# Optimization experiments

Hardware: AMD Instinct MI355X
Metric: run time of the kernel (lower is better)

## Reference

```python
import jax, jax.numpy as jnp
import numpy as np

F_DIM, HID, H, DQ, DV = 1024, 4096, 16, 64, 64
EPS = 1e-6

def layer_norm(x, w, b):
    mu = jnp.mean(x, axis=-1, keepdims=True)
    var = jnp.mean(jnp.square(x - mu), axis=-1, keepdims=True)
    return (x - mu) * jax.lax.rsqrt(var + EPS) * w + b

def setup_inputs() -> dict:
    key = jax.random.key(0)
    ks = jax.random.split(key, 8)
    s = 0.02
    return {
        'x': jax.random.normal(ks[0], (4, 2048, F_DIM), dtype=jnp.float32),
        'ln1_w': jnp.ones((F_DIM,), jnp.float32),
        'ln1_b': jnp.zeros((F_DIM,), jnp.float32),
        'wq_w': jax.random.normal(ks[1], (H * DQ, F_DIM), jnp.float32) * s,
        'wq_b': jnp.zeros((H * DQ,), jnp.float32),
        'wk_w': jax.random.normal(ks[2], (H * DQ, F_DIM), jnp.float32) * s,
        'wk_b': jnp.zeros((H * DQ,), jnp.float32),
        'wv_w': jax.random.normal(ks[3], (H * DV, F_DIM), jnp.float32) * s,
        'wv_b': jnp.zeros((H * DV,), jnp.float32),
        'fc_w': jax.random.normal(ks[4], (F_DIM, H * DV), jnp.float32) * s,
        'fc_b': jnp.zeros((F_DIM,), jnp.float32),
        'ln2_w': jnp.ones((F_DIM,), jnp.float32),
        'ln2_b': jnp.zeros((F_DIM,), jnp.float32),
        'fc1_w': jax.random.normal(ks[5], (HID, F_DIM), jnp.float32) * s,
        'fc1_b': jnp.zeros((HID,), jnp.float32),
        'fc2_w': jax.random.normal(ks[6], (F_DIM, HID), jnp.float32) * s,
        'fc2_b': jnp.zeros((F_DIM,), jnp.float32),
    }

def reference(x, ln1_w, ln1_b, wq_w, wq_b, wk_w, wk_b, wv_w, wv_b,
              fc_w, fc_b, ln2_w, ln2_b, fc1_w, fc1_b, fc2_w, fc2_b):
    B, S, _ = x.shape
    # --- pre-LN multi-head self-attention ---
    h = layer_norm(x, ln1_w, ln1_b)
    q = (h @ wq_w.T + wq_b).reshape(B, S, H, DQ).transpose(0, 2, 1, 3)  # [B,H,S,dq]
    k = (h @ wk_w.T + wk_b).reshape(B, S, H, DQ).transpose(0, 2, 1, 3)
    v = (h @ wv_w.T + wv_b).reshape(B, S, H, DV).transpose(0, 2, 1, 3)
    attn = jax.nn.softmax(jnp.einsum('bhqd,bhkd->bhqk', q, k) / jnp.sqrt(jnp.float32(DQ)), axis=-1)
    out = jnp.einsum('bhqk,bhkd->bhqd', attn, v).transpose(0, 2, 1, 3).reshape(B, S, H * DV)
    x = x + (out @ fc_w.T + fc_b)
    # --- pre-LN residual MLP ---
    h2 = layer_norm(x, ln2_w, ln2_b)
    ff = jax.nn.relu(h2 @ fc1_w.T + fc1_b) @ fc2_w.T + fc2_b
    return x + ff
```

## Files before the change

kernel.cpp:

```cpp
#include <hip/hip_runtime.h>

#define F_DIMC 1024
#define HIDC   4096
#define NH     16
#define SEQ    2048
#define BATCH  4
#define ROWS   (BATCH * SEQ)
#define MEG    (1u << 20)
#define QSCALE 0.18033688011112042f

typedef unsigned short u16t;
typedef __attribute__((ext_vector_type(8))) short short8;
typedef __attribute__((ext_vector_type(4))) float floatx4;
typedef __attribute__((address_space(1))) void gvoid_t;
typedef __attribute__((address_space(3))) void lvoid_t;
#define ASYNC16(g, l) __builtin_amdgcn_global_load_lds((gvoid_t*)(g), (lvoid_t*)(l), 16, 0, 0)

#if __has_builtin(__builtin_amdgcn_exp2f)
#define EXP2(x) __builtin_amdgcn_exp2f(x)
#else
#define EXP2(x) exp2f(x)
#endif

__device__ __forceinline__ u16t f2bf(float f) {
    union { float f; unsigned u; } v; v.f = f;
    unsigned r = v.u + 0x7fffu + ((v.u >> 16) & 1u);
    return (u16t)(r >> 16);
}
__device__ __forceinline__ unsigned fasu(float f) {
    union { float f; unsigned u; } v; v.f = f; return v.u;
}

__global__ __launch_bounds__(256) void ln_kernel(const float* __restrict__ x,
                                                 const float* __restrict__ w,
                                                 const float* __restrict__ b,
                                                 u16t* __restrict__ out) {
    const int row = blockIdx.x;
    const int t = threadIdx.x;
    const float* xp = x + (size_t)row * F_DIMC;

    float4 v = *(const float4*)(xp + t * 4);
    float s  = v.x + v.y + v.z + v.w;
    float ss = v.x * v.x + v.y * v.y + v.z * v.z + v.w * v.w;
    for (int off = 32; off; off >>= 1) {
        s  += __shfl_down(s, off);
        ss += __shfl_down(ss, off);
    }
    __shared__ float red[8];
    const int wid = t >> 6, lid = t & 63;
    if (lid == 0) { red[wid] = s; red[4 + wid] = ss; }
    __syncthreads();
    if (t == 0) {
        float S  = red[0] + red[1] + red[2] + red[3];
        float SS = red[4] + red[5] + red[6] + red[7];
        float mu  = S * (1.0f / F_DIMC);
        float var = SS * (1.0f / F_DIMC) - mu * mu;
        red[0] = mu;
        red[1] = rsqrtf(var + 1e-6f);
    }
    __syncthreads();
    const float mu = red[0], rs = red[1];

    float4 wv = *(const float4*)(w + t * 4);
    float4 bv = *(const float4*)(b + t * 4);
    ushort4 o = make_ushort4(f2bf((v.x - mu) * rs * wv.x + bv.x),
                             f2bf((v.y - mu) * rs * wv.y + bv.y),
                             f2bf((v.z - mu) * rs * wv.z + bv.z),
                             f2bf((v.w - mu) * rs * wv.w + bv.w));
    *(ushort4*)(out + (size_t)row * F_DIMC + t * 4) = o;
}

__global__ __launch_bounds__(256) void wconv_kernel(const float* __restrict__ w0,
        const float* __restrict__ w1, const float* __restrict__ w2,
        const float* __restrict__ w3, const float* __restrict__ w4,
        const float* __restrict__ w5, u16t* __restrict__ dst) {
    const size_t e = ((size_t)blockIdx.x * 256 + threadIdx.x) * 4;
    const float* src; size_t off;
    if      (e < 1 * MEG) { src = w0; off = e; }
    else if (e < 2 * MEG) { src = w1; off = e - 1 * MEG; }
    else if (e < 3 * MEG) { src = w2; off = e - 2 * MEG; }
    else if (e < 4 * MEG) { src = w3; off = e - 3 * MEG; }
    else if (e < 8 * MEG) { src = w4; off = e - 4 * MEG; }
    else                  { src = w5; off = e - 8 * MEG; }
    float4 f = *(const float4*)(src + off);
    *(ushort4*)(dst + e) = make_ushort4(f2bf(f.x), f2bf(f.y), f2bf(f.z), f2bf(f.w));
}

#define DP_CORE(Aq, Wq, Kdim)                                                  \
    __shared__ u16t As[3][128 * 64] __attribute__((aligned(16)));              \
    __shared__ u16t Bs[3][256 * 64] __attribute__((aligned(16)));              \
    const int t = threadIdx.x;                                                 \
    const int lane = t & 63;                                                   \
    const int wave = t >> 6;                                                   \
    const int wm = wave >> 2, wn = wave & 3;                                   \
    const int fm = lane & 15, fq = lane >> 4;                                  \
        \
    const int nwg = gridDim.x;                                                 \
    const int swzb = (blockIdx.x & 7) * (nwg >> 3) + (blockIdx.x >> 3);        \
    const int m0 = (swzb & 63) * 128;                \
    const int n0 = (swzb >> 6) * 256;                                          \
                \
    const u16t* ag[2]; int alo[2];                                             \
    _Pragma("unroll")                                                          \
    for (int i = 0; i < 2; ++i) {                                              \
        const int beta = i * 512 + t;                                          \
        const int r = beta >> 3, j = (beta & 7) ^ (r & 7);                     \
        ag[i] = (Aq) + (size_t)(m0 + r) * (Kdim) + j * 8;                      \
        alo[i] = beta * 8;                                                     \
    }                                                                          \
    const u16t* bg[4]; int blo[4];                                             \
    _Pragma("unroll")                                                          \
    for (int i = 0; i < 4; ++i) {                                              \
        const int beta = i * 512 + t;                                          \
        const int r = beta >> 3, j = (beta & 7) ^ (r & 7);                     \
        bg[i] = (Wq) + (size_t)(n0 + r) * (Kdim) + j * 8;                      \
        blo[i] = beta * 8;                                                     \
    }                                                                          \
                \
    int aoffk[2], boffk[2];                                                    \
    {                                                                          \
        const int ra0 = wm * 64 + fm, rb0 = wn * 64 + fm;                      \
        _Pragma("unroll")                                                      \
        for (int ks = 0; ks < 2; ++ks) {                                       \
            aoffk[ks] = ra0 * 64 + ((ks * 4 + fq) ^ (ra0 & 7)) * 8;            \
            boffk[ks] = rb0 * 64 + ((ks * 4 + fq) ^ (rb0 & 7)) * 8;            \
        }                                                                      \
    }                                                                          \
    const int NT = (Kdim) / 64;                                                \
                       \
    _Pragma("unroll")                                                          \
    for (int i = 0; i < 2; ++i) ASYNC16(ag[i], &As[0][alo[i]]);                \
    _Pragma("unroll")                                                          \
    for (int i = 0; i < 4; ++i) ASYNC16(bg[i], &Bs[0][blo[i]]);                \
    _Pragma("unroll")                                                          \
    for (int i = 0; i < 2; ++i) { ASYNC16(ag[i] + 64, &As[1][alo[i]]); ag[i] += 128; } \
    _Pragma("unroll")                                                          \
    for (int i = 0; i < 4; ++i) { ASYNC16(bg[i] + 64, &Bs[1][blo[i]]); bg[i] += 128; } \
    asm volatile("s_waitcnt vmcnt(6)" ::: "memory");         \
    __builtin_amdgcn_s_barrier();                                              \
    __builtin_amdgcn_sched_barrier(0);                                         \
    floatx4 acc[4][4] = {};                                                    \
    int sc = 0, ss = 2;                                                        \
    for (int tt = 0; tt < NT; ++tt) {                                          \
        const u16t* Ab = As[sc];                                               \
        const u16t* Bb = Bs[sc];                                               \
        if (tt + 2 < NT) {                \
            u16t* la = As[ss]; u16t* lb = Bs[ss];                              \
            _Pragma("unroll")                                                  \
            for (int i = 0; i < 2; ++i) { ASYNC16(ag[i], la + alo[i]); ag[i] += 64; } \
            _Pragma("unroll")                                                  \
            for (int i = 0; i < 4; ++i) { ASYNC16(bg[i], lb + blo[i]); bg[i] += 64; } \
        }                                                                      \
        short8 fb0[4], fa0[4], fb1[4], fa1[4];                                 \
        _Pragma("unroll")                                                      \
        for (int ni = 0; ni < 4; ++ni) fb0[ni] = *(const short8*)(Bb + boffk[0] + ni * 1024); \
        _Pragma("unroll")                                                      \
        for (int mi = 0; mi < 4; ++mi) fa0[mi] = *(const short8*)(Ab + aoffk[0] + mi * 1024); \
        _Pragma("unroll")                                                      \
        for (int ni = 0; ni < 4; ++ni) fb1[ni] = *(const short8*)(Bb + boffk[1] + ni * 1024); \
        _Pragma("unroll")                                                      \
        for (int mi = 0; mi < 4; ++mi) fa1[mi] = *(const short8*)(Ab + aoffk[1] + mi * 1024); \
        asm volatile("s_waitcnt lgkmcnt(8)" ::: "memory");   \
        __builtin_amdgcn_sched_barrier(0);                                     \
        __builtin_amdgcn_s_setprio(1);                                         \
        _Pragma("unroll")                                                      \
        for (int mi = 0; mi < 4; ++mi)                                         \
            _Pragma("unroll")                                                  \
            for (int ni = 0; ni < 4; ++ni)                                     \
                acc[mi][ni] = __builtin_amdgcn_mfma_f32_16x16x32_bf16(         \
                    fa0[mi], fb0[ni], acc[mi][ni], 0, 0, 0);                   \
        __builtin_amdgcn_s_setprio(0);                                         \
        asm volatile("s_waitcnt lgkmcnt(0)" ::: "memory");   \
        __builtin_amdgcn_sched_barrier(0);                                     \
                                       \
        if (tt + 2 < NT) { asm volatile("s_waitcnt vmcnt(6)" ::: "memory"); }  \
        else             { asm volatile("s_waitcnt vmcnt(0)" ::: "memory"); }  \
        __builtin_amdgcn_s_barrier();                                          \
        __builtin_amdgcn_sched_barrier(0);                                     \
        __builtin_amdgcn_s_setprio(1);                                         \
        _Pragma("unroll")                                                      \
        for (int mi = 0; mi < 4; ++mi)                                         \
            _Pragma("unroll")                                                  \
            for (int ni = 0; ni < 4; ++ni)                                     \
                acc[mi][ni] = __builtin_amdgcn_mfma_f32_16x16x32_bf16(         \
                    fa1[mi], fb1[ni], acc[mi][ni], 0, 0, 0);                   \
        __builtin_amdgcn_s_setprio(0);                                         \
        sc = sc == 2 ? 0 : sc + 1;                                             \
        ss = ss == 2 ? 0 : ss + 1;                                             \
    }

template <bool RELU, bool RES, bool BF16OUT>
__global__ __launch_bounds__(512, 2) void gemm_dp(const u16t* __restrict__ A,
                                                  const u16t* __restrict__ W,
                                                  const float* __restrict__ bias,
                                                  const float* res, void* Cout,
                                                  int N, int K) {
    DP_CORE(A, W, K)
    float bl[4];
#pragma unroll
    for (int ni = 0; ni < 4; ++ni) bl[ni] = bias[n0 + wn * 64 + ni * 16 + fm];
#pragma unroll
    for (int mi = 0; mi < 4; ++mi) {
#pragma unroll
        for (int ni = 0; ni < 4; ++ni) {
            const int col = n0 + wn * 64 + ni * 16 + fm;
#pragma unroll
            for (int r = 0; r < 4; ++r) {
                const int row = m0 + wm * 64 + mi * 16 + fq * 4 + r;
                const size_t off = (size_t)row * N + col;
                float c = acc[mi][ni][r] + bl[ni];
                if (RELU) c = fmaxf(c, 0.0f);
                if (RES)  c += res[off];
                if (BF16OUT) ((u16t*)Cout)[off] = f2bf(c);
                else         ((float*)Cout)[off] = c;
            }
        }
    }
}

__global__ __launch_bounds__(512, 2) void gemm_qkv(const u16t* __restrict__ A,
        const u16t* __restrict__ W,
        const float* __restrict__ wq_b, const float* __restrict__ wk_b,
        const float* __restrict__ wv_b,
        u16t* __restrict__ qb, u16t* __restrict__ kb, u16t* __restrict__ vtb) {
    DP_CORE(A, W, F_DIMC)
    const int which = n0 >> 10;
    const int nb = n0 & 1023;
    const float* bias = which == 0 ? wq_b : which == 1 ? wk_b : wv_b;
    float bl[4];
#pragma unroll
    for (int ni = 0; ni < 4; ++ni) bl[ni] = bias[nb + wn * 64 + ni * 16 + fm];

    if (which == 2) {
#pragma unroll
        for (int mi = 0; mi < 4; ++mi)
#pragma unroll
            for (int ni = 0; ni < 4; ++ni) {
                const int col = nb + wn * 64 + ni * 16 + fm;
                const int row0 = m0 + wm * 64 + mi * 16 + fq * 4;
                ushort4 pk = make_ushort4(f2bf(acc[mi][ni][0] + bl[ni]),
                                          f2bf(acc[mi][ni][1] + bl[ni]),
                                          f2bf(acc[mi][ni][2] + bl[ni]),
                                          f2bf(acc[mi][ni][3] + bl[ni]));
                *(ushort4*)(vtb + (size_t)col * ROWS + row0) = pk;
            }
    } else {
        u16t* dst = (which == 0) ? qb : kb;
        const float sc2 = (which == 0) ? QSCALE : 1.0f;
#pragma unroll
        for (int mi = 0; mi < 4; ++mi)
#pragma unroll
            for (int ni = 0; ni < 4; ++ni) {
                const int col = nb + wn * 64 + ni * 16 + fm;
#pragma unroll
                for (int r = 0; r < 4; ++r) {
                    const int row = m0 + wm * 64 + mi * 16 + fq * 4 + r;
                    dst[(size_t)row * F_DIMC + col] = f2bf((acc[mi][ni][r] + bl[ni]) * sc2);
                }
            }
    }
}

__global__ __launch_bounds__(256, 4) void attn_mfma(const u16t* __restrict__ qb,
        const u16t* __restrict__ kbuf, const u16t* __restrict__ vtb,
        u16t* __restrict__ ab) {
    __shared__ u16t Kt[2][64 * 64] __attribute__((aligned(16)));
    __shared__ u16t Vs[64 * 64] __attribute__((aligned(16)));
    __shared__ u16t QP[128 * 64] __attribute__((aligned(16)));

    const int t = threadIdx.x;
    const int lane = t & 63;
    const int wave = t >> 6;
    const int l15 = lane & 15, q4 = lane >> 4;
    const int q0 = blockIdx.x * 128;
    const int bh = blockIdx.y;
    const int b = bh >> 4, hh = bh & 15;

#pragma unroll
    for (int c = 0; c < 4; ++c) {
        const int beta = c * 256 + t;
        const int r = beta >> 3, o = (beta & 7) ^ (r & 7);
        ASYNC16(qb + (size_t)(b * SEQ + q0 + r) * F_DIMC + hh * 64 + o * 8,
                QP + beta * 8);
    }
    const u16t* kg = kbuf + (size_t)(b * SEQ) * F_DIMC + hh * 64;
    const u16t* vg = vtb + (size_t)(hh * 64) * ROWS + b * SEQ;

    const int sb0 = t, sb1 = t + 256;
    const int sr0 = sb0 >> 3, so0 = (sb0 & 7) ^ (sr0 & 7);
    const int sr1 = sb1 >> 3, so1 = (sb1 & 7) ^ (sr1 & 7);
    const u16t* kp0 = kg + (size_t)sr0 * F_DIMC + so0 * 8;
    const u16t* kp1 = kg + (size_t)sr1 * F_DIMC + so1 * 8;
    const u16t* vp0 = vg + (size_t)sr0 * ROWS + so0 * 8;
    const u16t* vp1 = vg + (size_t)sr1 * ROWS + so1 * 8;

    ASYNC16(kp0, Kt[0] + sb0 * 8);
    ASYNC16(kp1, Kt[0] + sb1 * 8);
    ASYNC16(vp0, Vs + sb0 * 8);
    ASYNC16(vp1, Vs + sb1 * 8);
    kp0 += 64 * F_DIMC; kp1 += 64 * F_DIMC; vp0 += 64; vp1 += 64;
    __syncthreads();

    short8 fqr[2][2];
#pragma unroll
    for (int mt = 0; mt < 2; ++mt)
#pragma unroll
        for (int ks = 0; ks < 2; ++ks) {
            const int m = wave * 32 + mt * 16 + l15;
            const int oct = ks * 4 + q4;
            fqr[mt][ks] = *(const short8*)(QP + (m * 8 + (oct ^ (m & 7))) * 8);
        }

    short8 ones;
#pragma unroll
    for (int i = 0; i < 8; ++i) ones[i] = (short)0x3F80;

    floatx4 oacc[2][4] = {};
    floatx4 lacc[2] = {};

    for (int it = 0; it < SEQ / 64; ++it) {
        if (it + 1 < SEQ / 64) {
            u16t* kd = Kt[(it + 1) & 1];
            ASYNC16(kp0, kd + sb0 * 8);
            ASYNC16(kp1, kd + sb1 * 8);
            kp0 += 64 * F_DIMC; kp1 += 64 * F_DIMC;
        }
        const u16t* kcur = Kt[it & 1];

        short8 fk[4][2];
#pragma unroll
        for (int nt = 0; nt < 4; ++nt)
#pragma unroll
            for (int ks = 0; ks < 2; ++ks) {
                const int kr = nt * 16 + l15;
                const int oct = ks * 4 + q4;
                fk[nt][ks] = *(const short8*)(kcur + (kr * 8 + (oct ^ (kr & 7))) * 8);
            }
        floatx4 st[2][4] = {};
#pragma unroll
        for (int mt = 0; mt < 2; ++mt)
#pragma unroll
            for (int nt = 0; nt < 4; ++nt) {
                st[mt][nt] = __builtin_amdgcn_mfma_f32_16x16x32_bf16(
                    fk[nt][0], fqr[mt][0], st[mt][nt], 0, 0, 0);
                st[mt][nt] = __builtin_amdgcn_mfma_f32_16x16x32_bf16(
                    fk[nt][1], fqr[mt][1], st[mt][nt], 0, 0, 0);
            }

#pragma unroll
        for (int mt = 0; mt < 2; ++mt)
#pragma unroll
            for (int nt = 0; nt < 4; ++nt) {
                const float p0 = EXP2(st[mt][nt][0]);
                const float p1 = EXP2(st[mt][nt][1]);
                const float p2 = EXP2(st[mt][nt][2]);
                const float p3 = EXP2(st[mt][nt][3]);
                const unsigned lo = __builtin_amdgcn_perm(fasu(p1), fasu(p0), 0x07060302u);
                const unsigned hi = __builtin_amdgcn_perm(fasu(p3), fasu(p2), 0x07060302u);
                const int m = wave * 32 + mt * 16 + l15;
                const int logb = nt * 2 + (q4 >> 1);
                *(uint2*)(QP + (m * 8 + (logb ^ (m & 7))) * 8 + (q4 & 1) * 4) =
                    make_uint2(lo, hi);
            }

        __syncthreads();

        short8 fp[2][2], fv[4][2];
#pragma unroll
        for (int mt = 0; mt < 2; ++mt)
#pragma unroll
            for (int ks = 0; ks < 2; ++ks) {
                const int m = wave * 32 + mt * 16 + l15;
                const int oct = ks * 4 + q4;
                fp[mt][ks] = *(const short8*)(QP + (m * 8 + (oct ^ (m & 7))) * 8);
            }
#pragma unroll
        for (int nd = 0; nd < 4; ++nd)
#pragma unroll
            for (int ks = 0; ks < 2; ++ks) {
                const int d = nd * 16 + l15;
                const int oct = ks * 4 + q4;
                fv[nd][ks] = *(const short8*)(Vs + (d * 8 + (oct ^ (d & 7))) * 8);
            }
#pragma unroll
        for (int mt = 0; mt < 2; ++mt) {
#pragma unroll
            for (int nd = 0; nd < 4; ++nd) {
                oacc[mt][nd] = __builtin_amdgcn_mfma_f32_16x16x32_bf16(
                    fp[mt][0], fv[nd][0], oacc[mt][nd], 0, 0, 0);
                oacc[mt][nd] = __builtin_amdgcn_mfma_f32_16x16x32_bf16(
                    fp[mt][1], fv[nd][1], oacc[mt][nd], 0, 0, 0);
            }
            lacc[mt] = __builtin_amdgcn_mfma_f32_16x16x32_bf16(
                fp[mt][0], ones, lacc[mt], 0, 0, 0);
            lacc[mt] = __builtin_amdgcn_mfma_f32_16x16x32_bf16(
                fp[mt][1], ones, lacc[mt], 0, 0, 0);
        }

        __syncthreads();
        if (it + 1 < SEQ / 64) {
            ASYNC16(vp0, Vs + sb0 * 8);
            ASYNC16(vp1, Vs + sb1 * 8);
            vp0 += 64; vp1 += 64;
        }
    }

#pragma unroll
    for (int mt = 0; mt < 2; ++mt) {
        floatx4 rinv;
#pragma unroll
        for (int r = 0; r < 4; ++r) rinv[r] = 1.0f / lacc[mt][r];
#pragma unroll
        for (int nd = 0; nd < 4; ++nd)
#pragma unroll
            for (int r = 0; r < 4; ++r) {
                const int row = b * SEQ + q0 + wave * 32 + mt * 16 + q4 * 4 + r;
                const int col = hh * 64 + nd * 16 + l15;
                ab[(size_t)row * F_DIMC + col] = f2bf(oacc[mt][nd][r] * rinv[r]);
            }
    }
}

extern "C" void kernel_launch(void* const* d_in, const int* in_sizes, int n_in,
                              void* d_out, int out_size, void* d_ws, size_t ws_size,
                              hipStream_t stream) {
    const float* x     = (const float*)d_in[0];
    const float* ln1_w = (const float*)d_in[1];
    const float* ln1_b = (const float*)d_in[2];
    const float* wq_w  = (const float*)d_in[3];
    const float* wq_b  = (const float*)d_in[4];
    const float* wk_w  = (const float*)d_in[5];
    const float* wk_b  = (const float*)d_in[6];
    const float* wv_w  = (const float*)d_in[7];
    const float* wv_b  = (const float*)d_in[8];
    const float* fc_w  = (const float*)d_in[9];
    const float* fc_b  = (const float*)d_in[10];
    const float* ln2_w = (const float*)d_in[11];
    const float* ln2_b = (const float*)d_in[12];
    const float* fc1_w = (const float*)d_in[13];
    const float* fc1_b = (const float*)d_in[14];
    const float* fc2_w = (const float*)d_in[15];
    const float* fc2_b = (const float*)d_in[16];

    float* out = (float*)d_out;
    u16t*  ws  = (u16t*)d_ws;

    u16t* wbuf = ws;
    u16t* bwqkv = wbuf;
    u16t* bwfc = wbuf + 3 * MEG;
    u16t* bwf1 = wbuf + 4 * MEG;
    u16t* bwf2 = wbuf + 8 * MEG;
    u16t* h    = wbuf + 12 * MEG;
    u16t* qb   = h + 8 * MEG;
    u16t* kb   = qb + 8 * MEG;
    u16t* vtb  = kb + 8 * MEG;
    u16t* ab   = vtb + 8 * MEG;
    u16t* ff   = qb;

    const dim3 blk(256);
    const dim3 blk512(512);
    const int gQKV = 64 * (3072 / 256);
    const int gF   = 64 * (F_DIMC / 256);
    const int gH   = 64 * (HIDC / 256);

    wconv_kernel<<<12 * MEG / 1024, blk, 0, stream>>>(wq_w, wk_w, wv_w, fc_w, fc1_w, fc2_w, wbuf);
    ln_kernel<<<ROWS, blk, 0, stream>>>(x, ln1_w, ln1_b, h);
    gemm_qkv<<<gQKV, blk512, 0, stream>>>(h, bwqkv, wq_b, wk_b, wv_b, qb, kb, vtb);
    attn_mfma<<<dim3(SEQ / 128, BATCH * NH), blk, 0, stream>>>(qb, kb, vtb, ab);
    gemm_dp<false, true, false><<<gF, blk512, 0, stream>>>(ab, bwfc, fc_b, x, out, F_DIMC, F_DIMC);
    ln_kernel<<<ROWS, blk, 0, stream>>>(out, ln2_w, ln2_b, h);
    gemm_dp<true, false, true><<<gH, blk512, 0, stream>>>(h, bwf1, fc1_b, nullptr, ff, HIDC, F_DIMC);
    gemm_dp<false, true, false><<<gF, blk512, 0, stream>>>(ff, bwf2, fc2_b, out, out, F_DIMC, HIDC);
}
```

Baseline: 565.0 us.

## Enlarge GEMM tiles to 256x256 with 8-wave ping-pong quarter-step pipeline

Replaces the 128x256 triple-buffered GEMM core with a 256x256 double-buffered core in which each wave computes a 128x64 output tile over four quarter-steps. Each quarter-step interleaves LDS fragment reads, async global-to-LDS loads for the next tiles, and MFMA bursts separated by barriers. The larger tile raises arithmetic intensity and halves the grid size. In exchange it uses more LDS (128KB) and accumulator registers, adds more barriers per K-step, and the grid becomes small for the N=1024 GEMMs (128 blocks), which may underfill the GPU.

```diff
diff --git a/kernel.cpp b/kernel.cpp
--- a/kernel.cpp
+++ b/kernel.cpp
@@ -86,107 +86,149 @@
     *(ushort4*)(dst + e) = make_ushort4(f2bf(f.x), f2bf(f.y), f2bf(f.z), f2bf(f.w));
 }
 
-#define DP_CORE(Aq, Wq, Kdim)                                                  \
-    __shared__ u16t As[3][128 * 64] __attribute__((aligned(16)));              \
-    __shared__ u16t Bs[3][256 * 64] __attribute__((aligned(16)));              \
+#define MFMA_Q(ACCM, ACCN, FA, FB)                                             \
+    _Pragma("unroll")                                                          \
+    for (int mi = 0; mi < 4; ++mi)                                             \
+        _Pragma("unroll")                                                      \
+        for (int ni = 0; ni < 2; ++ni) {                                       \
+            acc[(ACCM) + mi][(ACCN) + ni] =                                    \
+                __builtin_amdgcn_mfma_f32_16x16x32_bf16(                       \
+                    FA[mi][0], FB[ni][0], acc[(ACCM) + mi][(ACCN) + ni], 0, 0, 0); \
+            acc[(ACCM) + mi][(ACCN) + ni] =                                    \
+                __builtin_amdgcn_mfma_f32_16x16x32_bf16(                       \
+                    FA[mi][1], FB[ni][1], acc[(ACCM) + mi][(ACCN) + ni], 0, 0, 0); \
+        }
+
+#define DP8_CORE(Aq, Wq, Kdim)                                                 \
+    __shared__ u16t As[2][256 * 64] __attribute__((aligned(16)));              \
+    __shared__ u16t Bs[2][256 * 64] __attribute__((aligned(16)));              \
     const int t = threadIdx.x;                                                 \
     const int lane = t & 63;                                                   \
     const int wave = t >> 6;                                                   \
-    const int wm = wave >> 2, wn = wave & 3;                                   \
+    const int wr = wave >> 2, wc = wave & 3;                                   \
     const int fm = lane & 15, fq = lane >> 4;                                  \
-        \
     const int nwg = gridDim.x;                                                 \
     const int swzb = (blockIdx.x & 7) * (nwg >> 3) + (blockIdx.x >> 3);        \
-    const int m0 = (swzb & 63) * 128;                \
-    const int n0 = (swzb >> 6) * 256;                                          \
-                \
-    const u16t* ag[2]; int alo[2];                                             \
+    const int m0 = (swzb & 31) * 256;                \
+    const int n0 = (swzb >> 5) * 256;                                          \
+       \
+    const int beta0 = t, beta1 = t + 512;                                      \
+    const int r0 = beta0 >> 3, j0 = (beta0 & 7) ^ (r0 & 7);                    \
+    const int r1 = beta1 >> 3, j1 = (beta1 & 7) ^ (r1 & 7);                    \
+    const u16t* aP0 = (Aq) + (size_t)(m0 + r0) * (Kdim) + j0 * 8;              \
+    const u16t* aP1 = (Aq) + (size_t)(m0 + r1) * (Kdim) + j1 * 8;              \
+    const u16t* bP0 = (Wq) + (size_t)(n0 + r0) * (Kdim) + j0 * 8;              \
+    const u16t* bP1 = (Wq) + (size_t)(n0 + r1) * (Kdim) + j1 * 8;              \
+    const size_t aH = (size_t)128 * (Kdim);      \
+    const int l0 = beta0 * 8, l1 = beta1 * 8;                                  \
+        \
+    int aoff[2], boff[2];                                                      \
     _Pragma("unroll")                                                          \
-    for (int i = 0; i < 2; ++i) {                                              \
-        const int beta = i * 512 + t;                                          \
-        const int r = beta >> 3, j = (beta & 7) ^ (r & 7);                     \
-        ag[i] = (Aq) + (size_t)(m0 + r) * (Kdim) + j * 8;                      \
-        alo[i] = beta * 8;                                                     \
-    }                                                                          \
-    const u16t* bg[4]; int blo[4];                                             \
-    _Pragma("unroll")                                                          \
-    for (int i = 0; i < 4; ++i) {                                              \
-        const int beta = i * 512 + t;                                          \
-        const int r = beta >> 3, j = (beta & 7) ^ (r & 7);                     \
-        bg[i] = (Wq) + (size_t)(n0 + r) * (Kdim) + j * 8;                      \
-        blo[i] = beta * 8;                                                     \
-    }                                                                          \
-                \
-    int aoffk[2], boffk[2];                                                    \
-    {                                                                          \
-        const int ra0 = wm * 64 + fm, rb0 = wn * 64 + fm;                      \
-        _Pragma("unroll")                                                      \
-        for (int ks = 0; ks < 2; ++ks) {                                       \
-            aoffk[ks] = ra0 * 64 + ((ks * 4 + fq) ^ (ra0 & 7)) * 8;            \
-            boffk[ks] = rb0 * 64 + ((ks * 4 + fq) ^ (rb0 & 7)) * 8;            \
-        }                                                                      \
+    for (int ks = 0; ks < 2; ++ks) {                                           \
+        const int sw = ((ks * 4 + fq) ^ (fm & 7)) * 8;                         \
+        aoff[ks] = wr * 8192 + fm * 64 + sw;                                   \
+        boff[ks] = (wc >> 1) * 8192 + ((wc & 1) * 64 + fm) * 64 + sw;          \
     }                                                                          \
     const int NT = (Kdim) / 64;                                                \
-                       \
-    _Pragma("unroll")                                                          \
-    for (int i = 0; i < 2; ++i) ASYNC16(ag[i], &As[0][alo[i]]);                \
-    _Pragma("unroll")                                                          \
-    for (int i = 0; i < 4; ++i) ASYNC16(bg[i], &Bs[0][blo[i]]);                \
-    _Pragma("unroll")                                                          \
-    for (int i = 0; i < 2; ++i) { ASYNC16(ag[i] + 64, &As[1][alo[i]]); ag[i] += 128; } \
-    _Pragma("unroll")                                                          \
-    for (int i = 0; i < 4; ++i) { ASYNC16(bg[i] + 64, &Bs[1][blo[i]]); bg[i] += 128; } \
-    asm volatile("s_waitcnt vmcnt(6)" ::: "memory");         \
+                         \
+    { u16t* d = &As[0][0];    ASYNC16(aP0, d + l0); ASYNC16(aP1, d + l1); }    \
+    { u16t* d = &As[0][8192]; ASYNC16(aP0 + aH, d + l0); ASYNC16(aP1 + aH, d + l1); } \
+    { u16t* d = &Bs[0][0];    ASYNC16(bP0, d + l0); ASYNC16(bP1, d + l1); }    \
+    { u16t* d = &Bs[0][8192]; ASYNC16(bP0 + aH, d + l0); ASYNC16(bP1 + aH, d + l1); } \
+    { u16t* d = &Bs[1][0];    ASYNC16(bP0 + 64, d + l0); ASYNC16(bP1 + 64, d + l1); } \
+    { u16t* d = &Bs[1][8192]; ASYNC16(bP0 + aH + 64, d + l0); ASYNC16(bP1 + aH + 64, d + l1); } \
+    asm volatile("s_waitcnt vmcnt(4)" ::: "memory");         \
     __builtin_amdgcn_s_barrier();                                              \
     __builtin_amdgcn_sched_barrier(0);                                         \
-    floatx4 acc[4][4] = {};                                                    \
-    int sc = 0, ss = 2;                                                        \
-    for (int tt = 0; tt < NT; ++tt) {                                          \
-        const u16t* Ab = As[sc];                                               \
-        const u16t* Bb = Bs[sc];                                               \
-        if (tt + 2 < NT) {                \
-            u16t* la = As[ss]; u16t* lb = Bs[ss];                              \
-            _Pragma("unroll")                                                  \
-            for (int i = 0; i < 2; ++i) { ASYNC16(ag[i], la + alo[i]); ag[i] += 64; } \
-            _Pragma("unroll")                                                  \
-            for (int i = 0; i < 4; ++i) { ASYNC16(bg[i], lb + blo[i]); bg[i] += 64; } \
-        }                                                                      \
-        short8 fb0[4], fa0[4], fb1[4], fa1[4];                                 \
+    floatx4 acc[8][4] = {};                                                    \
+    short8 fa[4][2], fbL[2][2], fbH[2][2];                                     \
+    for (int T = 0; T < NT; ++T) {                                             \
+        const u16t* Ab = &As[T & 1][0];                                        \
+        const u16t* Bb = &Bs[T & 1][0];                                        \
+        const size_t kA = (size_t)(T + 1) * 64;                                \
+        const size_t kB = (size_t)(T + 2) * 64;                                \
+                                    \
         _Pragma("unroll")                                                      \
-        for (int ni = 0; ni < 4; ++ni) fb0[ni] = *(const short8*)(Bb + boffk[0] + ni * 1024); \
+        for (int mi = 0; mi < 4; ++mi) {                                       \
+            fa[mi][0] = *(const short8*)(Ab + aoff[0] + mi * 1024);            \
+            fa[mi][1] = *(const short8*)(Ab + aoff[1] + mi * 1024);            \
+        }                                                                      \
         _Pragma("unroll")                                                      \
-        for (int mi = 0; mi < 4; ++mi) fa0[mi] = *(const short8*)(Ab + aoffk[0] + mi * 1024); \
+        for (int ni = 0; ni < 2; ++ni) {                                       \
+            fbL[ni][0] = *(const short8*)(Bb + boff[0] + ni * 1024);           \
+            fbL[ni][1] = *(const short8*)(Bb + boff[1] + ni * 1024);           \
+        }                                                                      \
+        __builtin_amdgcn_sched_barrier(0);                                     \
+        if (T + 1 < NT) {                                                      \
+            u16t* d = &As[(T + 1) & 1][0];                                     \
+            ASYNC16(aP0 + kA, d + l0); ASYNC16(aP1 + kA, d + l1);              \
+        }                                                                      \
+        asm volatile("s_waitcnt lgkmcnt(8)" ::: "memory");                     \
+        __builtin_amdgcn_sched_barrier(0);                                     \
+        __builtin_amdgcn_s_barrier();                                          \
+        asm volatile("s_waitcnt lgkmcnt(0)" ::: "memory");                     \
+        __builtin_amdgcn_sched_barrier(0);                                     \
+        __builtin_amdgcn_s_setprio(1);                                         \
+        MFMA_Q(0, 0, fa, fbL)                                                  \
+        __builtin_amdgcn_s_setprio(0);                                         \
+        __builtin_amdgcn_sched_barrier(0);                                     \
+        __builtin_amdgcn_s_barrier();                                          \
+                                    \
         _Pragma("unroll")                                                      \
-        for (int ni = 0; ni < 4; ++ni) fb1[ni] = *(const short8*)(Bb + boffk[1] + ni * 1024); \
+        for (int ni = 0; ni < 2; ++ni) {                                       \
+            fbH[ni][0] = *(const short8*)(Bb + boff[0] + 2048 + ni * 1024);    \
+            fbH[ni][1] = *(const short8*)(Bb + boff[1] + 2048 + ni * 1024);    \
+        }                                                                      \
+        __builtin_amdgcn_sched_barrier(0);                                     \
+        if (T + 1 < NT) {                                                      \
+            u16t* d = &As[(T + 1) & 1][8192];                                  \
+            ASYNC16(aP0 + aH + kA, d + l0); ASYNC16(aP1 + aH + kA, d + l1);    \
+        }                                                                      \
+        __builtin_amdgcn_sched_barrier(0);                                     \
+        __builtin_amdgcn_s_barrier();                                          \
+        asm volatile("s_waitcnt lgkmcnt(0)" ::: "memory");                     \
+        __builtin_amdgcn_sched_barrier(0);                                     \
+        __builtin_amdgcn_s_setprio(1);                                         \
+        MFMA_Q(0, 2, fa, fbH)                                                  \
+        __builtin_amdgcn_s_setprio(0);                                         \
+        __builtin_amdgcn_sched_barrier(0);                                     \
+        __builtin_amdgcn_s_barrier();                                          \
+                                    \
         _Pragma("unroll")                                                      \
-        for (int mi = 0; mi < 4; ++mi) fa1[mi] = *(const short8*)(Ab + aoffk[1] + mi * 1024); \
-        asm volatile("s_waitcnt lgkmcnt(8)" ::: "memory");   \
+        for (int mi = 0; mi < 4; ++mi) {                                       \
+            fa[mi][0] = *(const short8*)(Ab + aoff[0] + 4096 + mi * 1024);     \
+            fa[mi][1] = *(const short8*)(Ab + aoff[1] + 4096 + mi * 1024);     \
+        }                                                                      \
+        __builtin_amdgcn_sched_barrier(0);                                     \
+        if (T + 2 < NT) {                                                      \
+            u16t* d = &Bs[T & 1][0];                                           \
+            ASYNC16(bP0 + kB, d + l0); ASYNC16(bP1 + kB, d + l1);              \
+        }                                                                      \
+        __builtin_amdgcn_sched_barrier(0);                                     \
+        __builtin_amdgcn_s_barrier();                                          \
+        asm volatile("s_waitcnt lgkmcnt(0)" ::: "memory");                     \
         __builtin_amdgcn_sched_barrier(0);                                     \
         __builtin_amdgcn_s_setprio(1);                                         \
-        _Pragma("unroll")                                                      \
-        for (int mi = 0; mi < 4; ++mi)                                         \
-            _Pragma("unroll")                                                  \
-            for (int ni = 0; ni < 4; ++ni)                                     \
-                acc[mi][ni] = __builtin_amdgcn_mfma_f32_16x16x32_bf16(         \
-                    fa0[mi], fb0[ni], acc[mi][ni], 0, 0, 0);                   \
+        MFMA_Q(4, 0, fa, fbL)                                                  \
         __builtin_amdgcn_s_setprio(0);                                         \
-        asm volatile("s_waitcnt lgkmcnt(0)" ::: "memory");   \
-        __builtin_amdgcn_sched_barrier(0);                                     \
-                                       \
-        if (tt + 2 < NT) { asm volatile("s_waitcnt vmcnt(6)" ::: "memory"); }  \
-        else             { asm volatile("s_waitcnt vmcnt(0)" ::: "memory"); }  \
+        __builtin_amdgcn_sched_barrier(0);                                     \
+        __builtin_amdgcn_s_barrier();                                          \
+                                    \
+        if (T + 2 < NT) {                                                      \
+            u16t* d = &Bs[T & 1][8192];                                        \
+            ASYNC16(bP0 + aH + kB, d + l0); ASYNC16(bP1 + aH + kB, d + l1);    \
+            asm volatile("s_waitcnt vmcnt(4)" ::: "memory");                   \
+        } else {                                                               \
+            asm volatile("s_waitcnt vmcnt(0)" ::: "memory");                   \
+        }                                                                      \
+        __builtin_amdgcn_sched_barrier(0);                                     \
         __builtin_amdgcn_s_barrier();                                          \
         __builtin_amdgcn_sched_barrier(0);                                     \
         __builtin_amdgcn_s_setprio(1);                                         \
-        _Pragma("unroll")                                                      \
-        for (int mi = 0; mi < 4; ++mi)                                         \
-            _Pragma("unroll")                                                  \
-            for (int ni = 0; ni < 4; ++ni)                                     \
-                acc[mi][ni] = __builtin_amdgcn_mfma_f32_16x16x32_bf16(         \
-                    fa1[mi], fb1[ni], acc[mi][ni], 0, 0, 0);                   \
+        MFMA_Q(4, 2, fa, fbH)                                                  \
         __builtin_amdgcn_s_setprio(0);                                         \
-        sc = sc == 2 ? 0 : sc + 1;                                             \
-        ss = ss == 2 ? 0 : ss + 1;                                             \
+        __builtin_amdgcn_sched_barrier(0);                                     \
+        __builtin_amdgcn_s_barrier();                                          \
     }
 
 template <bool RELU, bool RES, bool BF16OUT>
@@ -195,18 +237,18 @@
                                                   const float* __restrict__ bias,
                                                   const float* res, void* Cout,
                                                   int N, int K) {
-    DP_CORE(A, W, K)
+    DP8_CORE(A, W, K)
     float bl[4];
 #pragma unroll
-    for (int ni = 0; ni < 4; ++ni) bl[ni] = bias[n0 + wn * 64 + ni * 16 + fm];
-#pragma unroll
-    for (int mi = 0; mi < 4; ++mi) {
+    for (int ni = 0; ni < 4; ++ni) bl[ni] = bias[n0 + wc * 64 + ni * 16 + fm];
+#pragma unroll
+    for (int mi = 0; mi < 8; ++mi) {
 #pragma unroll
         for (int ni = 0; ni < 4; ++ni) {
-            const int col = n0 + wn * 64 + ni * 16 + fm;
+            const int col = n0 + wc * 64 + ni * 16 + fm;
 #pragma unroll
             for (int r = 0; r < 4; ++r) {
-                const int row = m0 + wm * 64 + mi * 16 + fq * 4 + r;
+                const int row = m0 + wr * 128 + mi * 16 + fq * 4 + r;
                 const size_t off = (size_t)row * N + col;
                 float c = acc[mi][ni][r] + bl[ni];
                 if (RELU) c = fmaxf(c, 0.0f);
@@ -223,21 +265,21 @@
         const float* __restrict__ wq_b, const float* __restrict__ wk_b,
         const float* __restrict__ wv_b,
         u16t* __restrict__ qb, u16t* __restrict__ kb, u16t* __restrict__ vtb) {
-    DP_CORE(A, W, F_DIMC)
+    DP8_CORE(A, W, F_DIMC)
     const int which = n0 >> 10;
     const int nb = n0 & 1023;
     const float* bias = which == 0 ? wq_b : which == 1 ? wk_b : wv_b;
     float bl[4];
 #pragma unroll
-    for (int ni = 0; ni < 4; ++ni) bl[ni] = bias[nb + wn * 64 + ni * 16 + fm];
+    for (int ni = 0; ni < 4; ++ni) bl[ni] = bias[nb + wc * 64 + ni * 16 + fm];
 
     if (which == 2) {
 #pragma unroll
-        for (int mi = 0; mi < 4; ++mi)
+        for (int mi = 0; mi < 8; ++mi)
 #pragma unroll
             for (int ni = 0; ni < 4; ++ni) {
-                const int col = nb + wn * 64 + ni * 16 + fm;
-                const int row0 = m0 + wm * 64 + mi * 16 + fq * 4;
+                const int col = nb + wc * 64 + ni * 16 + fm;
+                const int row0 = m0 + wr * 128 + mi * 16 + fq * 4;
                 ushort4 pk = make_ushort4(f2bf(acc[mi][ni][0] + bl[ni]),
                                           f2bf(acc[mi][ni][1] + bl[ni]),
                                           f2bf(acc[mi][ni][2] + bl[ni]),
@@ -248,13 +290,13 @@
         u16t* dst = (which == 0) ? qb : kb;
         const float sc2 = (which == 0) ? QSCALE : 1.0f;
 #pragma unroll
-        for (int mi = 0; mi < 4; ++mi)
+        for (int mi = 0; mi < 8; ++mi)
 #pragma unroll
             for (int ni = 0; ni < 4; ++ni) {
-                const int col = nb + wn * 64 + ni * 16 + fm;
+                const int col = nb + wc * 64 + ni * 16 + fm;
 #pragma unroll
                 for (int r = 0; r < 4; ++r) {
-                    const int row = m0 + wm * 64 + mi * 16 + fq * 4 + r;
+                    const int row = m0 + wr * 128 + mi * 16 + fq * 4 + r;
                     dst[(size_t)row * F_DIMC + col] = f2bf((acc[mi][ni][r] + bl[ni]) * sc2);
                 }
             }
@@ -459,9 +501,9 @@
 
     const dim3 blk(256);
     const dim3 blk512(512);
-    const int gQKV = 64 * (3072 / 256);
-    const int gF   = 64 * (F_DIMC / 256);
-    const int gH   = 64 * (HIDC / 256);
+    const int gQKV = 32 * (3072 / 256);
+    const int gF   = 32 * (F_DIMC / 256);
+    const int gH   = 32 * (HIDC / 256);
 
     wconv_kernel<<<12 * MEG / 1024, blk, 0, stream>>>(wq_w, wk_w, wv_w, fc_w, fc1_w, fc2_w, wbuf);
     ln_kernel<<<ROWS, blk, 0, stream>>>(x, ln1_w, ln1_b, h);
```

Result: no change. 567.5 us (+0.4%).
